# Performance work log

Measured on AMD Instinct MI355X. Metric: run time of the kernel, lower is better.

## Reference

```python
import jax, jax.numpy as jnp
import numpy as np

IN_U = 1024
OUT_U = 1024
BATCH = 4096
HID = 20            # ceil(log2(IN_U*OUT_U)), layer_encoding_dim=0 since num_layers=1
MLP_H = 10
FEAT = 3 + 3 * HID  # 63


def setup_inputs() -> dict:
    key = jax.random.key(0)
    ks = jax.random.split(key, 6)
    X = jax.random.normal(ks[0], (BATCH, IN_U), dtype=jnp.float32)
    weight = jax.random.normal(ks[1], (IN_U, OUT_U), dtype=jnp.float32) * 0.02
    # binary positional encodings per cell (encode_weight_hidden_states)
    k = jnp.arange(IN_U * OUT_U, dtype=jnp.int32).reshape(IN_U, OUT_U)
    shifts = jnp.arange(HID - 1, -1, -1, dtype=jnp.int32)
    hidden = ((k[..., None] >> shifts) & 1).astype(jnp.float32)  # [IN_U, OUT_U, HID]
    W1 = jax.random.normal(ks[2], (FEAT, MLP_H), dtype=jnp.float32) / np.float32(np.sqrt(FEAT))
    b1 = jnp.zeros((MLP_H,), jnp.float32)
    W2 = jax.random.normal(ks[3], (MLP_H, MLP_H), dtype=jnp.float32) / np.float32(np.sqrt(MLP_H))
    b2 = jnp.zeros((MLP_H,), jnp.float32)
    W3 = jax.random.normal(ks[4], (MLP_H, 1 + HID), dtype=jnp.float32) / np.float32(np.sqrt(MLP_H))
    b3 = jnp.zeros((1 + HID,), jnp.float32)
    return {"X": X, "weight": weight, "hidden": hidden,
            "W1": W1, "b1": b1, "W2": W2, "b2": b2, "W3": W3, "b3": b3}


def reference(X, weight, hidden, W1, b1, W2, b2, W3, b3):
    n, m = weight.shape
    # exclude-self column means ('forward') and row means ('backward')
    fwd_mean = (jnp.sum(weight, axis=0, keepdims=True) - weight) / (n - 1)   # [n,m]
    bwd_mean = (jnp.sum(weight, axis=1, keepdims=True) - weight) / (m - 1)   # [n,m]
    fwd_hs = (jnp.sum(hidden, axis=0, keepdims=True) - hidden) / (n - 1)     # [n,m,H]
    bwd_hs = (jnp.sum(hidden, axis=1, keepdims=True) - hidden) / (m - 1)     # [n,m,H]
    feat = jnp.concatenate(
        [weight[..., None], fwd_mean[..., None], bwd_mean[..., None],
         hidden, fwd_hs, bwd_hs], axis=-1)                                   # [n,m,3+3H]
    h = jax.nn.relu(jnp.einsum('nmf,fh->nmh', feat, W1) + b1)
    h = jax.nn.relu(jnp.einsum('nmh,hk->nmk', h, W2) + b2)
    updates = jnp.einsum('nmk,ko->nmo', h, W3) + b3                          # [n,m,1+H]
    new_weight = weight + updates[..., 0]
    # (hidden states also get updates[...,1:] in the torch module, but only the
    #  softmax output is returned)
    logits = jax.nn.relu(X @ new_weight)                                     # [B,m]
    return jax.nn.softmax(logits, axis=-1)
```

## Files before the change

### kernel.cpp

```cpp
#include <hip/hip_runtime.h>
#include <hip/hip_bf16.h>
#include <stdint.h>


typedef __attribute__((ext_vector_type(8))) short bf16x8;
typedef __attribute__((ext_vector_type(4))) float f32x4;

__device__ __forceinline__ unsigned short f2bf_rn(float x) {
    unsigned u = __float_as_uint(x);
    return (unsigned short)((u + 0x7fffu + ((u >> 16) & 1u)) >> 16);
}
__device__ __forceinline__ float bf2f(unsigned short h) {
    return __uint_as_float(((unsigned)h) << 16);
}
__device__ __forceinline__ void gld16(const void* g, void* l) {
    __builtin_amdgcn_global_load_lds(
        (const __attribute__((address_space(1))) unsigned*)g,
        (__attribute__((address_space(3))) unsigned*)l, 16, 0, 0);
}

__global__ __launch_bounds__(256) void k_sums2(const float* __restrict__ w,
                                               float* __restrict__ rs,
                                               float* __restrict__ cs) {
    __shared__ float part[4][1024];
    int t = threadIdx.x, lane = t & 63, wv = t >> 6;
    int row = blockIdx.x * 4 + wv;
    float rsum = 0.f;
    #pragma unroll
    for (int j = 0; j < 16; ++j) {
        float v = w[(size_t)row * 1024 + j * 64 + lane];
        part[wv][j * 64 + lane] = v;
        rsum += v;
    }
    #pragma unroll
    for (int o = 32; o; o >>= 1) rsum += __shfl_down(rsum, o);
    if (lane == 0) rs[row] = rsum;
    __syncthreads();
    #pragma unroll
    for (int j = 0; j < 4; ++j) {
        int c = t + j * 256;
        atomicAdd(&cs[c], part[0][c] + part[1][c] + part[2][c] + part[3][c]);
    }
}

__global__ void k_tables(const float* __restrict__ rs, const float* __restrict__ cs,
                         const float* __restrict__ W1, const float* __restrict__ b1,
                         float* __restrict__ rn, float* __restrict__ cm) {
    int id = blockIdx.x * 256 + threadIdx.x;
    if (id >= 2048) return;
    int n = id & 1023;
    int side = id >> 10;
    const float inv = 1.0f / 1023.0f;
    if (side == 0) {
        float r = rs[n];
        for (int h = 0; h < 10; h++) {
            float v = r * W1[2 * 10 + h] * inv;
            for (int j = 0; j < 10; j++) {
                float bit = (float)((n >> (9 - j)) & 1);
                v += bit * (W1[(3 + j) * 10 + h] + W1[(43 + j) * 10 + h]
                            - W1[(23 + j) * 10 + h] * inv);
                v += (512.0f * inv) * W1[(23 + j) * 10 + h];
            }
            rn[n * 10 + h] = v;
        }
    } else {
        float c = cs[n];
        for (int h = 0; h < 10; h++) {
            float v = c * W1[1 * 10 + h] * inv + b1[h];
            for (int j = 0; j < 10; j++) {
                float bit = (float)((n >> (9 - j)) & 1);
                v += bit * (W1[(13 + j) * 10 + h] + W1[(33 + j) * 10 + h]
                            - W1[(53 + j) * 10 + h] * inv);
                v += (512.0f * inv) * W1[(53 + j) * 10 + h];
            }
            cm[n * 10 + h] = v;
        }
    }
}

__global__ __launch_bounds__(256) void k_nw(const float* __restrict__ w,
        const float* __restrict__ rn, const float* __restrict__ cm,
        const float* __restrict__ W1, const float* __restrict__ W2,
        const float* __restrict__ b2, const float* __restrict__ W3,
        const float* __restrict__ b3, unsigned short* __restrict__ Bt) {
    __shared__ float sW2[100], sb2[10], sw3[10], sa[10];
    __shared__ float s_rn[320], s_cm[320];
    __shared__ float st[32][33];
    int t = threadIdx.x;
    int n0 = blockIdx.x * 32;
    int m0 = blockIdx.y * 32;
    for (int i = t; i < 320; i += 256) { s_rn[i] = rn[n0 * 10 + i]; s_cm[i] = cm[m0 * 10 + i]; }
    if (t < 100) sW2[t] = W2[t];
    if (t < 10) {
        sb2[t] = b2[t];
        sw3[t] = W3[t * 21];
        sa[t]  = W1[t] - (W1[10 + t] + W1[20 + t]) * (1.0f / 1023.0f);
    }
    float b30 = b3[0];
    __syncthreads();
    int ml = t & 31;
    #pragma unroll
    for (int i = 0; i < 4; i++) {
        int nl = (t >> 5) + 8 * i;
        float wv = w[(size_t)(n0 + nl) * 1024 + m0 + ml];
        float h1[10];
        #pragma unroll
        for (int h = 0; h < 10; h++)
            h1[h] = fmaxf(wv * sa[h] + s_rn[nl * 10 + h] + s_cm[ml * 10 + h], 0.f);
        float u = b30;
        #pragma unroll
        for (int k = 0; k < 10; k++) {
            float h2 = sb2[k];
            #pragma unroll
            for (int h = 0; h < 10; h++) h2 += h1[h] * sW2[h * 10 + k];
            u += fmaxf(h2, 0.f) * sw3[k];
        }
        st[nl][ml] = wv + u;
    }
    __syncthreads();
    int mrow = t >> 3, kc = t & 7;
    unsigned short hi4[4], lo4[4];
    #pragma unroll
    for (int j = 0; j < 4; j++) {
        float v = st[kc * 4 + j][mrow];
        unsigned short h = f2bf_rn(v);
        hi4[j] = h;
        lo4[j] = f2bf_rn(v - bf2f(h));
    }
    size_t base = (size_t)(m0 + mrow) * 2048 + n0 + kc * 4;
    *(ushort4*)&Bt[base]        = make_ushort4(hi4[0], hi4[1], hi4[2], hi4[3]);
    *(ushort4*)&Bt[base + 1024] = make_ushort4(lo4[0], lo4[1], lo4[2], lo4[3]);
}

__global__ __launch_bounds__(256) void k_convX(const float* __restrict__ X,
        unsigned short* __restrict__ Ah, unsigned short* __restrict__ Al) {
    size_t idx = ((size_t)blockIdx.x * 256 + threadIdx.x) * 4;
    float4 v = *(const float4*)&X[idx];
    ushort4 h, l;
    h.x = f2bf_rn(v.x); l.x = f2bf_rn(v.x - bf2f(h.x));
    h.y = f2bf_rn(v.y); l.y = f2bf_rn(v.y - bf2f(h.y));
    h.z = f2bf_rn(v.z); l.z = f2bf_rn(v.z - bf2f(h.z));
    h.w = f2bf_rn(v.w); l.w = f2bf_rn(v.w - bf2f(h.w));
    *(ushort4*)&Ah[idx] = h;
    *(ushort4*)&Al[idx] = l;
}

__global__ __launch_bounds__(256, 1) void k_gemm3(const unsigned short* __restrict__ Ah,
        const unsigned short* __restrict__ Al, const unsigned short* __restrict__ Bt,
        float* __restrict__ out) {
    __shared__ unsigned short sAh[128 * 64], sAl[128 * 64];
    __shared__ unsigned short sBh[128 * 64], sBl[128 * 64];
    int tid = threadIdx.x;
    int lane = tid & 63, w = tid >> 6;
    int n0 = blockIdx.x * 128, m0 = blockIdx.y * 128;
    int wm = (w >> 1) * 64, wn = (w & 1) * 64;
    int quad = lane >> 4, l16 = lane & 15;

    f32x4 acc[4][4];
    #pragma unroll
    for (int i = 0; i < 4; i++)
        #pragma unroll
        for (int j = 0; j < 4; j++) acc[i][j] = (f32x4)0.f;

    for (int it = 0; it < 16; ++it) {
        int kb = it * 64;
        __syncthreads();
        #pragma unroll
        for (int s = 0; s < 4; ++s) {
            int P = s * 256 + tid;
            int row = P >> 3;
            int seg = (P & 7) ^ (row & 7);
            int ldsOff = (s * 256 + w * 64) * 8;
            size_t ga = (size_t)(m0 + row) * 1024 + kb + seg * 8;
            size_t gb = (size_t)(n0 + row) * 2048 + kb + seg * 8;
            gld16(&Ah[ga], &sAh[ldsOff]);
            gld16(&Al[ga], &sAl[ldsOff]);
            gld16(&Bt[gb], &sBh[ldsOff]);
            gld16(&Bt[gb + 1024], &sBl[ldsOff]);
        }
        __syncthreads();
        #pragma unroll
        for (int ks = 0; ks < 2; ++ks) {
            int segk = ks * 4 + quad;
            bf16x8 ah[4], al[4], bh[4], bl[4];
            #pragma unroll
            for (int i = 0; i < 4; ++i) {
                int ra = wm + i * 16 + l16;
                int ca = (ra * 8 + (segk ^ (ra & 7))) * 8;
                ah[i] = *(const bf16x8*)&sAh[ca];
                al[i] = *(const bf16x8*)&sAl[ca];
                int rb = wn + i * 16 + l16;
                int cb = (rb * 8 + (segk ^ (rb & 7))) * 8;
                bh[i] = *(const bf16x8*)&sBh[cb];
                bl[i] = *(const bf16x8*)&sBl[cb];
            }
            #pragma unroll
            for (int i = 0; i < 4; ++i)
                #pragma unroll
                for (int j = 0; j < 4; ++j) {
                    acc[i][j] = __builtin_amdgcn_mfma_f32_16x16x32_bf16(ah[i], bh[j], acc[i][j], 0, 0, 0);
                    acc[i][j] = __builtin_amdgcn_mfma_f32_16x16x32_bf16(al[i], bh[j], acc[i][j], 0, 0, 0);
                    acc[i][j] = __builtin_amdgcn_mfma_f32_16x16x32_bf16(ah[i], bl[j], acc[i][j], 0, 0, 0);
                }
        }
    }
    #pragma unroll
    for (int i = 0; i < 4; ++i) {
        int mr = m0 + wm + i * 16 + quad * 4;
        #pragma unroll
        for (int j = 0; j < 4; ++j) {
            int nc = n0 + wn + j * 16 + l16;
            #pragma unroll
            for (int r = 0; r < 4; ++r)
                out[(size_t)(mr + r) * 1024 + nc] = fmaxf(acc[i][j][r], 0.f);
        }
    }
}

__global__ __launch_bounds__(256) void k_softmax2(float* __restrict__ C) {
    int row = blockIdx.x, t = threadIdx.x, lane = t & 63, wv = t >> 6;
    __shared__ float red[8];
    float4 v = *(float4*)&C[(size_t)row * 1024 + t * 4];
    float lm = fmaxf(fmaxf(v.x, v.y), fmaxf(v.z, v.w));
    #pragma unroll
    for (int o = 32; o; o >>= 1) lm = fmaxf(lm, __shfl_down(lm, o));
    if (lane == 0) red[wv] = lm;
    __syncthreads();
    float mx = fmaxf(fmaxf(red[0], red[1]), fmaxf(red[2], red[3]));
    float4 e;
    e.x = __expf(v.x - mx); e.y = __expf(v.y - mx);
    e.z = __expf(v.z - mx); e.w = __expf(v.w - mx);
    float ls = e.x + e.y + e.z + e.w;
    #pragma unroll
    for (int o = 32; o; o >>= 1) ls += __shfl_down(ls, o);
    if (lane == 0) red[4 + wv] = ls;
    __syncthreads();
    float inv = 1.0f / (red[4] + red[5] + red[6] + red[7]);
    e.x *= inv; e.y *= inv; e.z *= inv; e.w *= inv;
    *(float4*)&C[(size_t)row * 1024 + t * 4] = e;
}

__global__ void k_newweight_f(const float* __restrict__ w,
                              const float* __restrict__ rn, const float* __restrict__ cm,
                              const float* __restrict__ W1, const float* __restrict__ W2,
                              const float* __restrict__ b2, const float* __restrict__ W3,
                              const float* __restrict__ b3, float* __restrict__ Wn) {
    __shared__ float sW2[100], sb2[10], sw3[10], sa[10], srn[10];
    int t = threadIdx.x;
    int g = blockIdx.x * 256 + t;
    int n = g >> 10, m = g & 1023;
    if (t < 100) sW2[t] = W2[t];
    if (t >= 128 && t < 138) sb2[t - 128] = b2[t - 128];
    if (t >= 160 && t < 170) sw3[t - 160] = W3[(t - 160) * 21];
    if (t >= 192 && t < 202) {
        int h = t - 192;
        sa[h] = W1[h] - (W1[10 + h] + W1[20 + h]) * (1.0f / 1023.0f);
    }
    if (t >= 224 && t < 234) { int h = t - 224; srn[h] = rn[n * 10 + h]; }
    __syncthreads();
    float wv = w[g];
    float h1[10];
    #pragma unroll
    for (int h = 0; h < 10; h++)
        h1[h] = fmaxf(wv * sa[h] + srn[h] + cm[m * 10 + h], 0.0f);
    float u = b3[0];
    #pragma unroll
    for (int k = 0; k < 10; k++) {
        float h2 = sb2[k];
        #pragma unroll
        for (int h = 0; h < 10; h++) h2 += h1[h] * sW2[h * 10 + k];
        u += fmaxf(h2, 0.0f) * sw3[k];
    }
    Wn[g] = wv + u;
}

__global__ __launch_bounds__(256) void k_gemm_f(const float* __restrict__ A,
                                                const float* __restrict__ B,
                                                float* __restrict__ C) {
    __shared__ float sA[16 * 132];
    __shared__ float sB[16 * 64];
    int tid = threadIdx.x;
    int tx = tid & 15, ty = tid >> 4;
    int n0 = blockIdx.x * 64, m0 = blockIdx.y * 128;
    float acc[8][4];
    #pragma unroll
    for (int i = 0; i < 8; i++)
        #pragma unroll
        for (int j = 0; j < 4; j++) acc[i][j] = 0.f;
    for (int k0 = 0; k0 < 1024; k0 += 16) {
        __syncthreads();
        #pragma unroll
        for (int s = 0; s < 2; s++) {
            int f = tid + 256 * s;
            int row = f >> 2, cseg = f & 3;
            const float4 v = *(const float4*)&A[(m0 + row) * 1024 + k0 + cseg * 4];
            sA[(cseg * 4 + 0) * 132 + row] = v.x;
            sA[(cseg * 4 + 1) * 132 + row] = v.y;
            sA[(cseg * 4 + 2) * 132 + row] = v.z;
            sA[(cseg * 4 + 3) * 132 + row] = v.w;
        }
        {
            int row = tid >> 4, cseg = tid & 15;
            *(float4*)&sB[row * 64 + cseg * 4] =
                *(const float4*)&B[(k0 + row) * 1024 + n0 + cseg * 4];
        }
        __syncthreads();
        #pragma unroll
        for (int kk = 0; kk < 16; kk++) {
            float4 a0 = *(const float4*)&sA[kk * 132 + ty * 8];
            float4 a1 = *(const float4*)&sA[kk * 132 + ty * 8 + 4];
            float4 bv = *(const float4*)&sB[kk * 64 + tx * 4];
            float av[8] = {a0.x, a0.y, a0.z, a0.w, a1.x, a1.y, a1.z, a1.w};
            float bb[4] = {bv.x, bv.y, bv.z, bv.w};
            #pragma unroll
            for (int i = 0; i < 8; i++)
                #pragma unroll
                for (int j = 0; j < 4; j++) acc[i][j] += av[i] * bb[j];
        }
    }
    #pragma unroll
    for (int i = 0; i < 8; i++) {
        float4 r;
        r.x = fmaxf(acc[i][0], 0.f);
        r.y = fmaxf(acc[i][1], 0.f);
        r.z = fmaxf(acc[i][2], 0.f);
        r.w = fmaxf(acc[i][3], 0.f);
        *(float4*)&C[(m0 + ty * 8 + i) * 1024 + n0 + tx * 4] = r;
    }
}

extern "C" void kernel_launch(void* const* d_in, const int* in_sizes, int n_in,
                              void* d_out, int out_size, void* d_ws, size_t ws_size,
                              hipStream_t stream) {
    const float* X  = (const float*)d_in[0];
    const float* W  = (const float*)d_in[1];
    const float* W1 = (const float*)d_in[3];
    const float* b1 = (const float*)d_in[4];
    const float* W2 = (const float*)d_in[5];
    const float* b2 = (const float*)d_in[6];
    const float* W3 = (const float*)d_in[7];
    const float* b3 = (const float*)d_in[8];

    float* ws = (float*)d_ws;
    float* rs = ws;
    float* cs = ws + 1024;
    float* rn = ws + 2048;
    float* cm = ws + 12288;
    float* out = (float*)d_out;

    hipMemsetAsync(cs, 0, 1024 * sizeof(float), stream);
    k_sums2<<<256, 256, 0, stream>>>(W, rs, cs);
    k_tables<<<8, 256, 0, stream>>>(rs, cs, W1, b1, rn, cm);

    const size_t NEED = 98304 + 4194304 + 2 * 8388608;
    if (ws_size >= NEED) {
        unsigned short* Bt = (unsigned short*)((char*)d_ws + 98304);
        unsigned short* Ah = (unsigned short*)((char*)d_ws + 98304 + 4194304);
        unsigned short* Al = Ah + (size_t)4096 * 1024;
        k_nw<<<dim3(32, 32), 256, 0, stream>>>(W, rn, cm, W1, W2, b2, W3, b3, Bt);
        k_convX<<<4096, 256, 0, stream>>>(X, Ah, Al);
        k_gemm3<<<dim3(8, 32), 256, 0, stream>>>(Ah, Al, Bt, out);
    } else {
        float* Wn = ws + 24576;
        k_newweight_f<<<4096, 256, 0, stream>>>(W, rn, cm, W1, W2, b2, W3, b3, Wn);
        k_gemm_f<<<dim3(16, 32), 256, 0, stream>>>(X, Wn, out);
    }
    k_softmax2<<<4096, 256, 0, stream>>>(out);
}
```

Measured before the change: 212.0 us.

## Fuse preprocessing kernels and drop memset, atomics and table kernel

Merges the weight row/column sum kernel and the X bf16 hi/lo split into one k_pre launch. Column sums go to per-block partial buffers instead of atomics, so the memset is no longer needed. The rn/cm table computation moves into k_nw, where each block rebuilds its own 32-row slices from rs and the cs partials. This removes two launches, a memset and the atomic contention. In exchange every k_nw block redundantly sums 64 partials and recomputes its table slices, and the fallback fp32 path for small workspaces is removed.

```diff
diff --git a/kernel.cpp b/kernel.cpp
--- a/kernel.cpp
+++ b/kernel.cpp
@@ -2,6 +2,12 @@
 #include <hip/hip_bf16.h>
 #include <stdint.h>
 
+
+#define RS_OFF      0
+#define CSPART_OFF  4096
+#define BT_OFF      266240
+#define AH_OFF      4460544
+#define AL_OFF      12849152
 
 typedef __attribute__((ext_vector_type(8))) short bf16x8;
 typedef __attribute__((ext_vector_type(4))) float f32x4;
@@ -19,84 +25,113 @@
         (__attribute__((address_space(3))) unsigned*)l, 16, 0, 0);
 }
 
-__global__ __launch_bounds__(256) void k_sums2(const float* __restrict__ w,
-                                               float* __restrict__ rs,
-                                               float* __restrict__ cs) {
-    __shared__ float part[4][1024];
-    int t = threadIdx.x, lane = t & 63, wv = t >> 6;
-    int row = blockIdx.x * 4 + wv;
-    float rsum = 0.f;
-    #pragma unroll
-    for (int j = 0; j < 16; ++j) {
-        float v = w[(size_t)row * 1024 + j * 64 + lane];
-        part[wv][j * 64 + lane] = v;
-        rsum += v;
-    }
-    #pragma unroll
-    for (int o = 32; o; o >>= 1) rsum += __shfl_down(rsum, o);
-    if (lane == 0) rs[row] = rsum;
-    __syncthreads();
-    #pragma unroll
-    for (int j = 0; j < 4; ++j) {
-        int c = t + j * 256;
-        atomicAdd(&cs[c], part[0][c] + part[1][c] + part[2][c] + part[3][c]);
-    }
-}
-
-__global__ void k_tables(const float* __restrict__ rs, const float* __restrict__ cs,
-                         const float* __restrict__ W1, const float* __restrict__ b1,
-                         float* __restrict__ rn, float* __restrict__ cm) {
-    int id = blockIdx.x * 256 + threadIdx.x;
-    if (id >= 2048) return;
-    int n = id & 1023;
-    int side = id >> 10;
-    const float inv = 1.0f / 1023.0f;
-    if (side == 0) {
-        float r = rs[n];
-        for (int h = 0; h < 10; h++) {
-            float v = r * W1[2 * 10 + h] * inv;
-            for (int j = 0; j < 10; j++) {
-                float bit = (float)((n >> (9 - j)) & 1);
-                v += bit * (W1[(3 + j) * 10 + h] + W1[(43 + j) * 10 + h]
-                            - W1[(23 + j) * 10 + h] * inv);
-                v += (512.0f * inv) * W1[(23 + j) * 10 + h];
-            }
-            rn[n * 10 + h] = v;
+__global__ __launch_bounds__(256) void k_pre(const float* __restrict__ w,
+        const float* __restrict__ X, float* __restrict__ rs,
+        float* __restrict__ cs_part,
+        unsigned short* __restrict__ Ah, unsigned short* __restrict__ Al) {
+    int t = threadIdx.x;
+    if (blockIdx.x < 64) {
+        __shared__ float part[4][1024];
+        int lane = t & 63, wv = t >> 6;
+        int r0 = blockIdx.x * 16 + wv * 4;
+        float ccol[16];
+        #pragma unroll
+        for (int j = 0; j < 16; ++j) ccol[j] = 0.f;
+        #pragma unroll
+        for (int rr = 0; rr < 4; ++rr) {
+            int row = r0 + rr;
+            float rsum = 0.f;
+            #pragma unroll
+            for (int j = 0; j < 16; ++j) {
+                float v = w[(size_t)row * 1024 + j * 64 + lane];
+                ccol[j] += v;
+                rsum += v;
+            }
+            #pragma unroll
+            for (int o = 32; o; o >>= 1) rsum += __shfl_down(rsum, o);
+            if (lane == 0) rs[row] = rsum;
+        }
+        #pragma unroll
+        for (int j = 0; j < 16; ++j) part[wv][j * 64 + lane] = ccol[j];
+        __syncthreads();
+        #pragma unroll
+        for (int j = 0; j < 4; ++j) {
+            int c = t + j * 256;
+            cs_part[(size_t)blockIdx.x * 1024 + c] =
+                part[0][c] + part[1][c] + part[2][c] + part[3][c];
         }
     } else {
-        float c = cs[n];
-        for (int h = 0; h < 10; h++) {
-            float v = c * W1[1 * 10 + h] * inv + b1[h];
-            for (int j = 0; j < 10; j++) {
-                float bit = (float)((n >> (9 - j)) & 1);
-                v += bit * (W1[(13 + j) * 10 + h] + W1[(33 + j) * 10 + h]
-                            - W1[(53 + j) * 10 + h] * inv);
-                v += (512.0f * inv) * W1[(53 + j) * 10 + h];
-            }
-            cm[n * 10 + h] = v;
+        int b2 = blockIdx.x - 64;
+        #pragma unroll
+        for (int p = 0; p < 4; ++p) {
+            size_t idx = (size_t)b2 * 4096 + p * 1024 + t * 4;
+            float4 v = *(const float4*)&X[idx];
+            ushort4 h, l;
+            h.x = f2bf_rn(v.x); l.x = f2bf_rn(v.x - bf2f(h.x));
+            h.y = f2bf_rn(v.y); l.y = f2bf_rn(v.y - bf2f(h.y));
+            h.z = f2bf_rn(v.z); l.z = f2bf_rn(v.z - bf2f(h.z));
+            h.w = f2bf_rn(v.w); l.w = f2bf_rn(v.w - bf2f(h.w));
+            *(ushort4*)&Ah[idx] = h;
+            *(ushort4*)&Al[idx] = l;
         }
     }
 }
 
 __global__ __launch_bounds__(256) void k_nw(const float* __restrict__ w,
-        const float* __restrict__ rn, const float* __restrict__ cm,
-        const float* __restrict__ W1, const float* __restrict__ W2,
-        const float* __restrict__ b2, const float* __restrict__ W3,
-        const float* __restrict__ b3, unsigned short* __restrict__ Bt) {
-    __shared__ float sW2[100], sb2[10], sw3[10], sa[10];
-    __shared__ float s_rn[320], s_cm[320];
+        const float* __restrict__ rs, const float* __restrict__ cs_part,
+        const float* __restrict__ W1, const float* __restrict__ b1,
+        const float* __restrict__ W2, const float* __restrict__ b2,
+        const float* __restrict__ W3, const float* __restrict__ b3,
+        unsigned short* __restrict__ Bt) {
+    __shared__ float sW1[630], sW2[100], sb1[10], sb2[10], sw3[10], sa[10];
+    __shared__ float rs_loc[32], cs_loc[32];
+    __shared__ float rn_loc[320], cm_loc[320];
     __shared__ float st[32][33];
     int t = threadIdx.x;
     int n0 = blockIdx.x * 32;
     int m0 = blockIdx.y * 32;
-    for (int i = t; i < 320; i += 256) { s_rn[i] = rn[n0 * 10 + i]; s_cm[i] = cm[m0 * 10 + i]; }
+    const float inv = 1.0f / 1023.0f;
+
+    for (int i = t; i < 630; i += 256) sW1[i] = W1[i];
     if (t < 100) sW2[t] = W2[t];
-    if (t < 10) {
-        sb2[t] = b2[t];
-        sw3[t] = W3[t * 21];
-        sa[t]  = W1[t] - (W1[10 + t] + W1[20 + t]) * (1.0f / 1023.0f);
+    if (t >= 128 && t < 138) { sb1[t - 128] = b1[t - 128]; sb2[t - 128] = b2[t - 128]; }
+    if (t >= 160 && t < 170) sw3[t - 160] = W3[(t - 160) * 21];
+    if (t >= 192 && t < 224) rs_loc[t - 192] = rs[n0 + t - 192];
+    if (t >= 224 && t < 256) {
+        float s = 0.f;
+        #pragma unroll
+        for (int p = 0; p < 64; ++p) s += cs_part[(size_t)p * 1024 + m0 + (t - 224)];
+        cs_loc[t - 224] = s;
     }
     float b30 = b3[0];
+    __syncthreads();
+    if (t < 10) sa[t] = sW1[t] - (sW1[10 + t] + sW1[20 + t]) * inv;
+    for (int id = t; id < 640; id += 256) {
+        int h = id % 10, i = (id / 10) & 31, side = id >= 320;
+        if (!side) {
+            int n = n0 + i;
+            float v = rs_loc[i] * sW1[20 + h] * inv;
+            #pragma unroll
+            for (int j = 0; j < 10; j++) {
+                float bit = (float)((n >> (9 - j)) & 1);
+                v += bit * (sW1[(3 + j) * 10 + h] + sW1[(43 + j) * 10 + h]
+                            - sW1[(23 + j) * 10 + h] * inv);
+                v += (512.0f * inv) * sW1[(23 + j) * 10 + h];
+            }
+            rn_loc[i * 10 + h] = v;
+        } else {
+            int m = m0 + i;
+            float v = cs_loc[i] * sW1[10 + h] * inv + sb1[h];
+            #pragma unroll
+            for (int j = 0; j < 10; j++) {
+                float bit = (float)((m >> (9 - j)) & 1);
+                v += bit * (sW1[(13 + j) * 10 + h] + sW1[(33 + j) * 10 + h]
+                            - sW1[(53 + j) * 10 + h] * inv);
+                v += (512.0f * inv) * sW1[(53 + j) * 10 + h];
+            }
+            cm_loc[i * 10 + h] = v;
+        }
+    }
     __syncthreads();
     int ml = t & 31;
     #pragma unroll
@@ -106,7 +141,7 @@
         float h1[10];
         #pragma unroll
         for (int h = 0; h < 10; h++)
-            h1[h] = fmaxf(wv * sa[h] + s_rn[nl * 10 + h] + s_cm[ml * 10 + h], 0.f);
+            h1[h] = fmaxf(wv * sa[h] + rn_loc[nl * 10 + h] + cm_loc[ml * 10 + h], 0.f);
         float u = b30;
         #pragma unroll
         for (int k = 0; k < 10; k++) {
@@ -130,19 +165,6 @@
     size_t base = (size_t)(m0 + mrow) * 2048 + n0 + kc * 4;
     *(ushort4*)&Bt[base]        = make_ushort4(hi4[0], hi4[1], hi4[2], hi4[3]);
     *(ushort4*)&Bt[base + 1024] = make_ushort4(lo4[0], lo4[1], lo4[2], lo4[3]);
-}
-
-__global__ __launch_bounds__(256) void k_convX(const float* __restrict__ X,
-        unsigned short* __restrict__ Ah, unsigned short* __restrict__ Al) {
-    size_t idx = ((size_t)blockIdx.x * 256 + threadIdx.x) * 4;
-    float4 v = *(const float4*)&X[idx];
-    ushort4 h, l;
-    h.x = f2bf_rn(v.x); l.x = f2bf_rn(v.x - bf2f(h.x));
-    h.y = f2bf_rn(v.y); l.y = f2bf_rn(v.y - bf2f(h.y));
-    h.z = f2bf_rn(v.z); l.z = f2bf_rn(v.z - bf2f(h.z));
-    h.w = f2bf_rn(v.w); l.w = f2bf_rn(v.w - bf2f(h.w));
-    *(ushort4*)&Ah[idx] = h;
-    *(ushort4*)&Al[idx] = l;
 }
 
 __global__ __launch_bounds__(256, 1) void k_gemm3(const unsigned short* __restrict__ Ah,
@@ -240,95 +262,6 @@
     *(float4*)&C[(size_t)row * 1024 + t * 4] = e;
 }
 
-__global__ void k_newweight_f(const float* __restrict__ w,
-                              const float* __restrict__ rn, const float* __restrict__ cm,
-                              const float* __restrict__ W1, const float* __restrict__ W2,
-                              const float* __restrict__ b2, const float* __restrict__ W3,
-                              const float* __restrict__ b3, float* __restrict__ Wn) {
-    __shared__ float sW2[100], sb2[10], sw3[10], sa[10], srn[10];
-    int t = threadIdx.x;
-    int g = blockIdx.x * 256 + t;
-    int n = g >> 10, m = g & 1023;
-    if (t < 100) sW2[t] = W2[t];
-    if (t >= 128 && t < 138) sb2[t - 128] = b2[t - 128];
-    if (t >= 160 && t < 170) sw3[t - 160] = W3[(t - 160) * 21];
-    if (t >= 192 && t < 202) {
-        int h = t - 192;
-        sa[h] = W1[h] - (W1[10 + h] + W1[20 + h]) * (1.0f / 1023.0f);
-    }
-    if (t >= 224 && t < 234) { int h = t - 224; srn[h] = rn[n * 10 + h]; }
-    __syncthreads();
-    float wv = w[g];
-    float h1[10];
-    #pragma unroll
-    for (int h = 0; h < 10; h++)
-        h1[h] = fmaxf(wv * sa[h] + srn[h] + cm[m * 10 + h], 0.0f);
-    float u = b3[0];
-    #pragma unroll
-    for (int k = 0; k < 10; k++) {
-        float h2 = sb2[k];
-        #pragma unroll
-        for (int h = 0; h < 10; h++) h2 += h1[h] * sW2[h * 10 + k];
-        u += fmaxf(h2, 0.0f) * sw3[k];
-    }
-    Wn[g] = wv + u;
-}
-
-__global__ __launch_bounds__(256) void k_gemm_f(const float* __restrict__ A,
-                                                const float* __restrict__ B,
-                                                float* __restrict__ C) {
-    __shared__ float sA[16 * 132];
-    __shared__ float sB[16 * 64];
-    int tid = threadIdx.x;
-    int tx = tid & 15, ty = tid >> 4;
-    int n0 = blockIdx.x * 64, m0 = blockIdx.y * 128;
-    float acc[8][4];
-    #pragma unroll
-    for (int i = 0; i < 8; i++)
-        #pragma unroll
-        for (int j = 0; j < 4; j++) acc[i][j] = 0.f;
-    for (int k0 = 0; k0 < 1024; k0 += 16) {
-        __syncthreads();
-        #pragma unroll
-        for (int s = 0; s < 2; s++) {
-            int f = tid + 256 * s;
-            int row = f >> 2, cseg = f & 3;
-            const float4 v = *(const float4*)&A[(m0 + row) * 1024 + k0 + cseg * 4];
-            sA[(cseg * 4 + 0) * 132 + row] = v.x;
-            sA[(cseg * 4 + 1) * 132 + row] = v.y;
-            sA[(cseg * 4 + 2) * 132 + row] = v.z;
-            sA[(cseg * 4 + 3) * 132 + row] = v.w;
-        }
-        {
-            int row = tid >> 4, cseg = tid & 15;
-            *(float4*)&sB[row * 64 + cseg * 4] =
-                *(const float4*)&B[(k0 + row) * 1024 + n0 + cseg * 4];
-        }
-        __syncthreads();
-        #pragma unroll
-        for (int kk = 0; kk < 16; kk++) {
-            float4 a0 = *(const float4*)&sA[kk * 132 + ty * 8];
-            float4 a1 = *(const float4*)&sA[kk * 132 + ty * 8 + 4];
-            float4 bv = *(const float4*)&sB[kk * 64 + tx * 4];
-            float av[8] = {a0.x, a0.y, a0.z, a0.w, a1.x, a1.y, a1.z, a1.w};
-            float bb[4] = {bv.x, bv.y, bv.z, bv.w};
-            #pragma unroll
-            for (int i = 0; i < 8; i++)
-                #pragma unroll
-                for (int j = 0; j < 4; j++) acc[i][j] += av[i] * bb[j];
-        }
-    }
-    #pragma unroll
-    for (int i = 0; i < 8; i++) {
-        float4 r;
-        r.x = fmaxf(acc[i][0], 0.f);
-        r.y = fmaxf(acc[i][1], 0.f);
-        r.z = fmaxf(acc[i][2], 0.f);
-        r.w = fmaxf(acc[i][3], 0.f);
-        *(float4*)&C[(m0 + ty * 8 + i) * 1024 + n0 + tx * 4] = r;
-    }
-}
-
 extern "C" void kernel_launch(void* const* d_in, const int* in_sizes, int n_in,
                               void* d_out, int out_size, void* d_ws, size_t ws_size,
                               hipStream_t stream) {
@@ -341,29 +274,16 @@
     const float* W3 = (const float*)d_in[7];
     const float* b3 = (const float*)d_in[8];
 
-    float* ws = (float*)d_ws;
-    float* rs = ws;
-    float* cs = ws + 1024;
-    float* rn = ws + 2048;
-    float* cm = ws + 12288;
+    char* wsb = (char*)d_ws;
+    float* rs            = (float*)(wsb + RS_OFF);
+    float* cs_part       = (float*)(wsb + CSPART_OFF);
+    unsigned short* Bt   = (unsigned short*)(wsb + BT_OFF);
+    unsigned short* Ah   = (unsigned short*)(wsb + AH_OFF);
+    unsigned short* Al   = (unsigned short*)(wsb + AL_OFF);
     float* out = (float*)d_out;
 
-    hipMemsetAsync(cs, 0, 1024 * sizeof(float), stream);
-    k_sums2<<<256, 256, 0, stream>>>(W, rs, cs);
-    k_tables<<<8, 256, 0, stream>>>(rs, cs, W1, b1, rn, cm);
-
-    const size_t NEED = 98304 + 4194304 + 2 * 8388608;
-    if (ws_size >= NEED) {
-        unsigned short* Bt = (unsigned short*)((char*)d_ws + 98304);
-        unsigned short* Ah = (unsigned short*)((char*)d_ws + 98304 + 4194304);
-        unsigned short* Al = Ah + (size_t)4096 * 1024;
-        k_nw<<<dim3(32, 32), 256, 0, stream>>>(W, rn, cm, W1, W2, b2, W3, b3, Bt);
-        k_convX<<<4096, 256, 0, stream>>>(X, Ah, Al);
-        k_gemm3<<<dim3(8, 32), 256, 0, stream>>>(Ah, Al, Bt, out);
-    } else {
-        float* Wn = ws + 24576;
-        k_newweight_f<<<4096, 256, 0, stream>>>(W, rn, cm, W1, W2, b2, W3, b3, Wn);
-        k_gemm_f<<<dim3(16, 32), 256, 0, stream>>>(X, Wn, out);
-    }
+    k_pre<<<1088, 256, 0, stream>>>(W, X, rs, cs_part, Ah, Al);
+    k_nw<<<dim3(32, 32), 256, 0, stream>>>(W, rs, cs_part, W1, b1, W2, b2, W3, b3, Bt);
+    k_gemm3<<<dim3(8, 32), 256, 0, stream>>>(Ah, Al, Bt, out);
     k_softmax2<<<4096, 256, 0, stream>>>(out);
 }
```

After: 202.1 us. 4.7% less time.
